# Kernel optimization log

Hardware: AMD Instinct MI355X
Metric: run time of the kernel (lower is better)

Reference implementation:

```python
import jax, jax.numpy as jnp
import numpy as np
from jax import lax

DN = ('NCHW', 'OIHW', 'NCHW')

def _conv(x, w, b, stride, pad):
    y = lax.conv_general_dilated(x, w, (stride, stride), ((pad, pad), (pad, pad)),
                                 dimension_numbers=DN)
    return y + b[None, :, None, None]

def _convT(x, w, b):
    # torch ConvTranspose2d(k=4, s=2, p=1); w: (C_in, C_out, 4, 4)
    wt = jnp.transpose(jnp.flip(w, (2, 3)), (1, 0, 2, 3))  # (C_out, C_in, 4, 4)
    y = lax.conv_general_dilated(x, wt, (1, 1), ((2, 2), (2, 2)),
                                 lhs_dilation=(2, 2), dimension_numbers=DN)
    return y + b[None, :, None, None]

def setup_inputs() -> dict:
    key = jax.random.key(0)
    ks = jax.random.split(key, 20)
    s = 0.05
    inp = {
        'x':   jax.random.normal(ks[0], (8, 1, 256, 256), jnp.float32),
        'ew1': jax.random.normal(ks[1], (64, 1, 3, 3), jnp.float32) * s,
        'eb1': jnp.zeros((64,), jnp.float32),
        'ew2': jax.random.normal(ks[2], (128, 64, 3, 3), jnp.float32) * s,
        'eb2': jnp.zeros((128,), jnp.float32),
        'ew3': jax.random.normal(ks[3], (256, 128, 3, 3), jnp.float32) * s,
        'eb3': jnp.zeros((256,), jnp.float32),
        'ew4': jax.random.normal(ks[4], (256, 256, 1, 1), jnp.float32) * s,
        'eb4': jnp.zeros((256,), jnp.float32),
        # torch init: uniform(-1/K, 1/K) with K=1024
        'codebook': jax.random.uniform(ks[5], (1024, 256), jnp.float32,
                                       minval=-1.0 / 1024, maxval=1.0 / 1024),
        'dw1': jax.random.normal(ks[6], (256, 256, 1, 1), jnp.float32) * s,
        'db1': jnp.zeros((256,), jnp.float32),
        'dw2': jax.random.normal(ks[7], (256, 128, 4, 4), jnp.float32) * s,
        'db2': jnp.zeros((128,), jnp.float32),
        'dw3': jax.random.normal(ks[8], (128, 64, 4, 4), jnp.float32) * s,
        'db3': jnp.zeros((64,), jnp.float32),
        'dw4': jax.random.normal(ks[9], (1, 64, 3, 3), jnp.float32) * s,
        'db4': jnp.zeros((1,), jnp.float32),
        'scale_idx': 2,
    }
    return inp

def reference(x, ew1, eb1, ew2, eb2, ew3, eb3, ew4, eb4, codebook,
              dw1, db1, dw2, db2, dw3, db3, dw4, db4, scale_idx):
    # ---- encoder (scale_idx=2: 1->64->128->256->embedding_dim) ----
    h = jax.nn.relu(_conv(x, ew1, eb1, 1, 1))        # [B,64,256,256]
    h = jax.nn.relu(_conv(h, ew2, eb2, 2, 1))        # [B,128,128,128]
    h = jax.nn.relu(_conv(h, ew3, eb3, 2, 1))        # [B,256,64,64]
    z = _conv(h, ew4, eb4, 1, 0)                     # [B,D,64,64]
    # ---- vector quantization ----
    B, D, H, W = z.shape
    flat = jnp.transpose(z, (0, 2, 3, 1)).reshape(-1, D)        # [N,D]
    dist = (jnp.sum(flat * flat, axis=1, keepdims=True)
            + jnp.sum(codebook * codebook, axis=1)
            - 2.0 * flat @ codebook.T)                          # [N,K]
    idx = jnp.argmin(dist, axis=1)                              # [N]
    quantized = codebook[idx].reshape(B, H, W, D)               # gather == onehot@codebook
    z_q = jnp.transpose(quantized, (0, 3, 1, 2))                # [B,D,H,W]
    indices = idx.reshape(B, H, W)
    # ---- decoder ----
    d = jax.nn.relu(_conv(z_q, dw1, db1, 1, 0))      # [B,256,64,64]
    d = jax.nn.relu(_convT(d, dw2, db2))             # [B,128,128,128]
    d = jax.nn.relu(_convT(d, dw3, db3))             # [B,64,256,256]
    recon = jax.nn.sigmoid(_conv(d, dw4, db4, 1, 1)) # [B,1,256,256]
    return recon, z_q, indices
```

## Files before the change

### kernel.cpp

```cpp
#include <hip/hip_runtime.h>
#include <hip/hip_bf16.h>
#include <math.h>


#define NB 8

typedef short v8s __attribute__((ext_vector_type(8)));
typedef float v4f __attribute__((ext_vector_type(4)));

__device__ __forceinline__ float sumsq128(const float* __restrict__ p, int stride) {
  float r[8];
#pragma unroll
  for (int j = 0; j < 8; ++j) {
    float v = p[(size_t)j * stride];
    r[j] = __fmul_rn(v, v);
  }
  for (int i = 8; i < 128; i += 8) {
#pragma unroll
    for (int j = 0; j < 8; ++j) {
      float v = p[(size_t)(i + j) * stride];
      r[j] = __fadd_rn(r[j], __fmul_rn(v, v));
    }
  }
  return __fadd_rn(__fadd_rn(__fadd_rn(r[0], r[1]), __fadd_rn(r[2], r[3])),
                   __fadd_rn(__fadd_rn(r[4], r[5]), __fadd_rn(r[6], r[7])));
}
__device__ __forceinline__ float sumsq256(const float* __restrict__ p, int stride) {
  return __fadd_rn(sumsq128(p, stride), sumsq128(p + (size_t)128 * stride, stride));
}

__global__ __launch_bounds__(256) void k_conv12(const float* __restrict__ x,
                                                const float* __restrict__ ew1,
                                                const float* __restrict__ eb1,
                                                const float* __restrict__ ew2,
                                                const float* __restrict__ bias2,
                                                float* __restrict__ out) {
  const int IH = 256;
  const int OH = 128;
  const int TILES_X = OH / 16;
  int n = blockIdx.z;
  int cg = blockIdx.y;
  int tile = blockIdx.x;
  int OY0 = (tile / TILES_X) * 16, OX0 = (tile % TILES_X) * 16;
  int ty = threadIdx.x >> 4, tx = threadIdx.x & 15;
  int oy = OY0 + ty, ox = OX0 + tx;

  const float* xin = x + (size_t)n * IH * IH;
  float xv[5][5];
#pragma unroll
  for (int a = 0; a < 5; ++a)
#pragma unroll
    for (int b = 0; b < 5; ++b) {
      int iy = 2 * oy - 2 + a, ix = 2 * ox - 2 + b;
      xv[a][b] = (iy >= 0 && iy < IH && ix >= 0 && ix < IH) ? xin[iy * IH + ix] : 0.f;
    }

  unsigned hmask = 0;
#pragma unroll
  for (int dy = 0; dy < 3; ++dy)
#pragma unroll
    for (int dx = 0; dx < 3; ++dx) {
      int hy = 2 * oy - 1 + dy, hx = 2 * ox - 1 + dx;
      if (hy >= 0 && hy < IH && hx >= 0 && hx < IH) hmask |= 1u << (dy * 3 + dx);
    }

  float acc[32];
#pragma unroll
  for (int c = 0; c < 32; ++c) acc[c] = 0.f;

  for (int ci = 0; ci < 64; ++ci) {
    const float* w1 = ew1 + ci * 9;
    float b1 = eb1[ci];
    float v[9];
#pragma unroll
    for (int dy = 0; dy < 3; ++dy)
#pragma unroll
      for (int dx = 0; dx < 3; ++dx) {
        int k = dy * 3 + dx;
        if (hmask & (1u << k)) {
          float h = b1;
#pragma unroll
          for (int ey = 0; ey < 3; ++ey)
#pragma unroll
            for (int ex = 0; ex < 3; ++ex) h += xv[dy + ey][dx + ex] * w1[ey * 3 + ex];
          v[k] = fmaxf(h, 0.f);
        } else {
          v[k] = 0.f;
        }
      }
    const float* wp = ew2 + ((size_t)(cg * 32) * 64 + ci) * 9;
#pragma unroll
    for (int c = 0; c < 32; ++c) {
#pragma unroll
      for (int k = 0; k < 9; ++k) acc[c] += v[k] * wp[(size_t)c * 64 * 9 + k];
    }
  }
  float* ob = out + (((size_t)n * 128 + cg * 32) * OH + oy) * OH + ox;
#pragma unroll
  for (int c = 0; c < 32; ++c) {
    float r = acc[c] + bias2[cg * 32 + c];
    ob[(size_t)c * OH * OH] = fmaxf(r, 0.f);
  }
}

template <int CI, int IH>
__global__ __launch_bounds__(256) void k_conv3s2(const float* __restrict__ in,
                                                 const float* __restrict__ w,
                                                 const float* __restrict__ bias,
                                                 float* __restrict__ out, int CO) {
  const int OH = IH / 2;
  const int TILES_X = OH / 16;
  const int RS = 40;
  int n = blockIdx.z;
  int cg = blockIdx.y;
  int tile = blockIdx.x;
  int OY0 = (tile / TILES_X) * 16, OX0 = (tile % TILES_X) * 16;
  int ty = threadIdx.x >> 4, tx = threadIdx.x & 15;
  __shared__ float sm[2][33 * RS];
  float acc[32];
#pragma unroll
  for (int c = 0; c < 32; ++c) acc[c] = 0.f;
  int iy0 = 2 * OY0 - 1, ix0 = 2 * OX0 - 1;
  const float* inb = in + (size_t)n * CI * IH * IH;

  for (int t = threadIdx.x; t < 2 * 33 * RS; t += 256) (&sm[0][0])[t] = 0.f;

  int goff[5], loff[5];
  unsigned vmask = 0;
#pragma unroll
  for (int i = 0; i < 5; ++i) {
    int t = threadIdx.x + 256 * i;
    if (t < 33 * 33) {
      int r = t / 33, c = t - r * 33;
      int iy = iy0 + r, ix = ix0 + c;
      if (iy >= 0 && iy < IH && ix >= 0 && ix < IH) {
        vmask |= 1u << i;
        goff[i] = iy * IH + ix;
        loff[i] = r * RS + (c >> 1) + (c & 1) * 17;
      }
    }
  }
  __syncthreads();

  auto stage = [&](int buf, int ci) {
    const float* ip = inb + (size_t)ci * IH * IH;
    float* dst = sm[buf];
#pragma unroll
    for (int i = 0; i < 5; ++i)
      if (vmask & (1u << i)) dst[loff[i]] = ip[goff[i]];
  };
  stage(0, 0);
  for (int ci = 0; ci < CI; ++ci) {
    int buf = ci & 1;
    __syncthreads();
    if (ci + 1 < CI) stage(buf ^ 1, ci + 1);
    float v[9];
#pragma unroll
    for (int dy = 0; dy < 3; ++dy)
#pragma unroll
      for (int dx = 0; dx < 3; ++dx)
        v[dy * 3 + dx] = sm[buf][(2 * ty + dy) * RS + (dx & 1) * 17 + tx + (dx >> 1)];
    const float* wp = w + ((size_t)(cg * 32) * CI + ci) * 9;
#pragma unroll
    for (int c = 0; c < 32; ++c) {
#pragma unroll
      for (int k = 0; k < 9; ++k) acc[c] += v[k] * wp[(size_t)c * CI * 9 + k];
    }
  }
  int oy = OY0 + ty, ox = OX0 + tx;
  float* ob = out + (((size_t)n * CO + cg * 32) * OH + oy) * OH + ox;
#pragma unroll
  for (int c = 0; c < 32; ++c) {
    float r = acc[c] + bias[cg * 32 + c];
    ob[(size_t)c * OH * OH] = fmaxf(r, 0.f);
  }
}

__global__ __launch_bounds__(256) void k_conv1x1(const float* __restrict__ in,
                                                 const float* __restrict__ w,
                                                 const float* __restrict__ bias,
                                                 float* __restrict__ out, int CI, int CO,
                                                 int HW) {
  int n = blockIdx.z;
  int cg = blockIdx.y;
  int px = blockIdx.x * 256 + threadIdx.x;
  __shared__ float sm[16][256];
  const float* inb = in + (size_t)n * CI * HW;
  float acc[8];
#pragma unroll
  for (int c = 0; c < 8; ++c) acc[c] = 0.f;
  for (int c0 = 0; c0 < CI; c0 += 16) {
#pragma unroll
    for (int i = 0; i < 16; ++i) sm[i][threadIdx.x] = inb[(size_t)(c0 + i) * HW + px];
    __syncthreads();
    const float* wb = w + (size_t)(cg * 8) * CI + c0;
#pragma unroll
    for (int i = 0; i < 16; ++i) {
      float r = sm[i][threadIdx.x];
#pragma unroll
      for (int c = 0; c < 8; ++c) acc[c] += r * wb[(size_t)c * CI + i];
    }
    __syncthreads();
  }
#pragma unroll
  for (int c = 0; c < 8; ++c) {
    float r = acc[c] + bias[cg * 8 + c];
    out[((size_t)n * CO + cg * 8 + c) * HW + px] = r;
  }
}

__global__ __launch_bounds__(256) void k_cnorm(const float* __restrict__ cb,
                                               float* __restrict__ cn) {
  int j = blockIdx.x * 256 + threadIdx.x;
  if (j < 1024) cn[j] = sumsq256(cb + (size_t)j * 256, 1);
}

__global__ __launch_bounds__(256) void k_xnorm(const float* __restrict__ z,
                                               float* __restrict__ xn) {
  int t = blockIdx.x * 256 + threadIdx.x;
  int n = t >> 12, yx = t & 4095;
  xn[t] = sumsq256(z + (size_t)n * 256 * 4096 + yx, 4096);
}

__global__ __launch_bounds__(256) void k_vq(const float* __restrict__ z,
                                            const float* __restrict__ cb,
                                            const float* __restrict__ cn,
                                            const float* __restrict__ xn,
                                            int* __restrict__ idx,
                                            float* __restrict__ idxf) {
  __shared__ __align__(16) float zt[64][68];
  __shared__ float ct[64][65];
  __shared__ float cnt[64];
  __shared__ float xnt[64];
  __shared__ float rbest[64][17];
  __shared__ int ribest[64][17];
  int tid = threadIdx.x;
  int pq = tid & 15;
  int cq = tid >> 4;
  int p0 = blockIdx.x * 64;
  int n = p0 >> 12;
  int yx0 = p0 & 4095;
  const float* zb = z + (size_t)n * 256 * 4096 + yx0;
  if (tid < 64) xnt[tid] = xn[p0 + tid];
  float best[4] = {3.0e38f, 3.0e38f, 3.0e38f, 3.0e38f};
  int bidx[4] = {0, 0, 0, 0};
  for (int c0 = 0; c0 < 1024; c0 += 64) {
    float acc[4][4];
#pragma unroll
    for (int a = 0; a < 4; ++a)
#pragma unroll
      for (int b = 0; b < 4; ++b) acc[a][b] = 0.f;
    for (int k0 = 0; k0 < 256; k0 += 64) {
      __syncthreads();
      for (int t = tid; t < 4096; t += 256) {
        int r = t >> 6, c = t & 63;
        zt[r][c] = zb[(size_t)(k0 + r) * 4096 + c];
      }
      for (int t = tid; t < 4096; t += 256) {
        int c = t >> 6, r = t & 63;
        ct[c][r] = cb[(size_t)(c0 + c) * 256 + k0 + r];
      }
      if (k0 == 0 && tid < 64) cnt[tid] = cn[c0 + tid];
      __syncthreads();
#pragma unroll 8
      for (int k = 0; k < 64; ++k) {
        const float4 zz = *reinterpret_cast<const float4*>(&zt[k][pq * 4]);
#pragma unroll
        for (int j = 0; j < 4; ++j) {
          float cv = ct[cq * 4 + j][k];
          acc[0][j] += zz.x * cv;
          acc[1][j] += zz.y * cv;
          acc[2][j] += zz.z * cv;
          acc[3][j] += zz.w * cv;
        }
      }
    }
#pragma unroll
    for (int pi = 0; pi < 4; ++pi) {
      float xnp = xnt[pq * 4 + pi];
#pragma unroll
      for (int j = 0; j < 4; ++j) {
        float A = __fadd_rn(xnp, cnt[cq * 4 + j]);
        float d = __fsub_rn(A, __fmul_rn(2.0f, acc[pi][j]));
        if (d < best[pi]) {
          best[pi] = d;
          bidx[pi] = c0 + cq * 4 + j;
        }
      }
    }
  }
  __syncthreads();
#pragma unroll
  for (int pi = 0; pi < 4; ++pi) {
    rbest[pq * 4 + pi][cq] = best[pi];
    ribest[pq * 4 + pi][cq] = bidx[pi];
  }
  __syncthreads();
  if (tid < 64) {
    float bv = rbest[tid][0];
    int bj = ribest[tid][0];
    for (int g = 1; g < 16; ++g) {
      float v = rbest[tid][g];
      int j2 = ribest[tid][g];
      if (v < bv || (v == bv && j2 < bj)) { bv = v; bj = j2; }
    }
    idx[p0 + tid] = bj;
    idxf[p0 + tid] = (float)bj;
  }
}

__global__ __launch_bounds__(256) void k_gather(const int* __restrict__ idx,
                                                const float* __restrict__ cb,
                                                float* __restrict__ zq,
                                                __hip_bfloat16* __restrict__ zqbf) {
  size_t t = (size_t)blockIdx.x * 256 + threadIdx.x;
  int yx = (int)(t & 4095);
  int d = (int)((t >> 12) & 255);
  int n = (int)(t >> 20);
  int p = (n << 12) | yx;
  float v = cb[(size_t)idx[p] * 256 + d];
  zq[t] = v;
  zqbf[t] = __float2bfloat16(v);
}

__global__ __launch_bounds__(256) void k_wconv(const float* __restrict__ w,
                                               __hip_bfloat16* __restrict__ wA,
                                               int CI, int CO) {
  int t = blockIdx.x * 256 + threadIdx.x;
  int total = 4 * CO * CI * 4;
  if (t >= total) return;
  int tap = t & 3;
  int q = t >> 2;
  int ci = q % CI;
  int pc = q / CI;
  int co = pc % CO;
  int par = pc / CO;
  int a = tap >> 1, b = tap & 1, ry = par >> 1, rx = par & 1;
  float v = w[((size_t)ci * CO + co) * 16 + (3 - ry - 2 * a) * 4 + (3 - rx - 2 * b)];
  wA[t] = __float2bfloat16(v);
}

__global__ __launch_bounds__(256) void k_wconv1(const float* __restrict__ w,
                                                __hip_bfloat16* __restrict__ wb) {
  int t = blockIdx.x * 256 + threadIdx.x;
  if (t < 65536) wb[t] = __float2bfloat16(w[t]);
}

__global__ __launch_bounds__(256) void k_d1mfma(const __hip_bfloat16* __restrict__ in,
                                                const __hip_bfloat16* __restrict__ wb,
                                                const float* __restrict__ bias,
                                                __hip_bfloat16* __restrict__ out) {
  int n = blockIdx.z;
  int co0 = blockIdx.y * 64;
  int px0 = blockIdx.x * 64;
  int tid = threadIdx.x;
  int w = tid >> 6, lane = tid & 63, fr = lane & 15, kg = lane >> 4;

  __shared__ __align__(16) ushort Wt[64][40];
  __shared__ __align__(16) ushort Zt[64][40];

  v4f acc[4];
#pragma unroll
  for (int q = 0; q < 4; ++q) acc[q] = (v4f){0.f, 0.f, 0.f, 0.f};

  const ushort* inb = (const ushort*)in + (size_t)n * 256 * 4096;
  const ushort* wab = (const ushort*)wb;

  for (int k0 = 0; k0 < 256; k0 += 32) {
    __syncthreads();
    {
      int co = tid & 63, kgg = tid >> 6;
      const uint4 v = *(const uint4*)(wab + (size_t)(co0 + co) * 256 + k0 + kgg * 8);
      *(uint4*)&Wt[co][kgg * 8] = v;
    }
    {
      int ci = tid >> 3, pxg = tid & 7;
      const ushort* src = inb + (size_t)(k0 + ci) * 4096 + px0 + pxg * 8;
      uint4 v = *(const uint4*)src;
      const ushort* vs = (const ushort*)&v;
#pragma unroll
      for (int j = 0; j < 8; ++j) Zt[pxg * 8 + j][ci] = vs[j];
    }
    __syncthreads();
    v8s af = *(const v8s*)&Wt[w * 16 + fr][kg * 8];
#pragma unroll
    for (int q = 0; q < 4; ++q) {
      v8s b = *(const v8s*)&Zt[q * 16 + fr][kg * 8];
      acc[q] = __builtin_amdgcn_mfma_f32_16x16x32_bf16(af, b, acc[q], 0, 0, 0);
    }
  }
  __hip_bfloat16* ob = out + (size_t)n * 256 * 4096;
#pragma unroll
  for (int q = 0; q < 4; ++q) {
    int px = px0 + q * 16 + fr;
#pragma unroll
    for (int r = 0; r < 4; ++r) {
      int co = co0 + w * 16 + kg * 4 + r;
      float val = fmaxf(acc[q][r] + bias[co], 0.f);
      ob[(size_t)co * 4096 + px] = __float2bfloat16(val);
    }
  }
}

template <int CI, int IH, int CO>
__global__ __launch_bounds__(256) void k_convTmfma(const __hip_bfloat16* __restrict__ in,
                                                   const __hip_bfloat16* __restrict__ wA,
                                                   const float* __restrict__ bias,
                                                   __hip_bfloat16* __restrict__ out) {
  const int OH = 2 * IH;
  const int NT = IH / 32;
  int n = blockIdx.z;
  int co0 = blockIdx.y * 64;
  int m = blockIdx.x / NT;
  int n0x = (blockIdx.x % NT) * 32;
  int tid = threadIdx.x;
  int w = tid >> 6, lane = tid & 63, fr = lane & 15, kg = lane >> 4;

  __shared__ __align__(16) ushort Wt[4][64][40];
  __shared__ __align__(16) ushort Bt[4][32][40];
  __shared__ ushort patch[8][3][36];

  v4f acc[4][2];
#pragma unroll
  for (int p = 0; p < 4; ++p)
#pragma unroll
    for (int h = 0; h < 2; ++h) acc[p][h] = (v4f){0.f, 0.f, 0.f, 0.f};

  const ushort* inb = (const ushort*)in + (size_t)n * CI * IH * IH;
  const ushort* wab = (const ushort*)wA;

  for (int t = tid; t < 8 * 3 * 36; t += 256) (&patch[0][0][0])[t] = 0;

  int pgoff[4], ploff[4];
  unsigned pmask = 0;
#pragma unroll
  for (int i = 0; i < 4; ++i) {
    int t = tid + 256 * i;
    if (t < 816) {
      int ci = t / 102;
      int rem = t - ci * 102;
      int r = rem / 34;
      int c = rem - r * 34;
      int iy = m - 1 + r, ix = n0x - 1 + c;
      if (iy >= 0 && iy < IH && ix >= 0 && ix < IH) {
        pmask |= 1u << i;
        pgoff[i] = (ci * IH + iy) * IH + ix;
        ploff[i] = (ci * 3 + r) * 36 + c;
      }
    }
  }

  for (int ci0 = 0; ci0 < CI; ci0 += 8) {
    __syncthreads();
    {
      const ushort* ip = inb + (size_t)ci0 * IH * IH;
      ushort* pb = &patch[0][0][0];
#pragma unroll
      for (int i = 0; i < 4; ++i)
        if (pmask & (1u << i)) pb[ploff[i]] = ip[pgoff[i]];
    }
#pragma unroll
    for (int i = 0; i < 4; ++i) {
      int u = tid + 256 * i;
      int kgg = u & 3, co = (u >> 2) & 63, par = u >> 8;
      const uint4 v =
          *(const uint4*)(wab + (((size_t)par * CO + co0 + co) * CI + ci0) * 4 + kgg * 8);
      *(uint4*)&Wt[par][co][kgg * 8] = v;
    }
    __syncthreads();
    {
      int pr = tid >> 1;
      int px0 = (tid & 1) * 16;
      int par = pr >> 5, k = pr & 31;
      int ci = k >> 2, a = (k >> 1) & 1, b = k & 1, ry = par >> 1, rx = par & 1;
      const ushort* src = &patch[ci][ry + a][px0 + rx + b];
      ushort* dst = &Bt[par][px0][k];
#pragma unroll
      for (int p = 0; p < 16; ++p) dst[p * 40] = src[p];
    }
    __syncthreads();
#pragma unroll
    for (int par = 0; par < 4; ++par) {
      v8s af = *(const v8s*)&Wt[par][w * 16 + fr][kg * 8];
      v8s b0 = *(const v8s*)&Bt[par][fr][kg * 8];
      v8s b1 = *(const v8s*)&Bt[par][16 + fr][kg * 8];
      acc[par][0] = __builtin_amdgcn_mfma_f32_16x16x32_bf16(af, b0, acc[par][0], 0, 0, 0);
      acc[par][1] = __builtin_amdgcn_mfma_f32_16x16x32_bf16(af, b1, acc[par][1], 0, 0, 0);
    }
  }
  __hip_bfloat16* ob = out + (size_t)n * CO * OH * OH;
#pragma unroll
  for (int par = 0; par < 4; ++par) {
    int ry = par >> 1, rx = par & 1;
    int oy = 2 * m + ry;
#pragma unroll
    for (int h = 0; h < 2; ++h) {
      int ox = 2 * (n0x + h * 16 + fr) + rx;
#pragma unroll
      for (int r = 0; r < 4; ++r) {
        int co = co0 + w * 16 + kg * 4 + r;
        float val = acc[par][h][r] + bias[co];
        val = fmaxf(val, 0.f);
        ob[((size_t)co * OH + oy) * OH + ox] = __float2bfloat16(val);
      }
    }
  }
}

__global__ __launch_bounds__(256) void k_conv_out(const __hip_bfloat16* __restrict__ in,
                                                  const float* __restrict__ w,
                                                  const float* __restrict__ bias,
                                                  float* __restrict__ out) {
  int n = blockIdx.z;
  int tile = blockIdx.x;
  int TY0 = (tile / 16) * 16, TX0 = (tile % 16) * 16;
  int ty = threadIdx.x >> 4, tx = threadIdx.x & 15;
  __shared__ float sm[2][18 * 18];
  float acc = bias[0];
  const __hip_bfloat16* inb = in + (size_t)n * 64 * 65536;
  int goff[2], loff[2];
  unsigned vmask = 0;
#pragma unroll
  for (int i = 0; i < 2; ++i) {
    int t = threadIdx.x + 256 * i;
    if (t < 324) {
      int r = t / 18, c = t - r * 18;
      int iy = TY0 - 1 + r, ix = TX0 - 1 + c;
      if (iy >= 0 && iy < 256 && ix >= 0 && ix < 256) {
        vmask |= 1u << i;
        goff[i] = iy * 256 + ix;
        loff[i] = t;
      }
    }
  }
  for (int t = threadIdx.x; t < 2 * 324; t += 256) (&sm[0][0])[t] = 0.f;
  __syncthreads();
  auto stage = [&](int buf, int ci) {
    const __hip_bfloat16* ip = inb + (size_t)ci * 65536;
    float* dst = sm[buf];
#pragma unroll
    for (int i = 0; i < 2; ++i)
      if (vmask & (1u << i)) dst[loff[i]] = __bfloat162float(ip[goff[i]]);
  };
  stage(0, 0);
  for (int ci = 0; ci < 64; ++ci) {
    int buf = ci & 1;
    __syncthreads();
    if (ci + 1 < 64) stage(buf ^ 1, ci + 1);
    const float* wp = w + ci * 9;
#pragma unroll
    for (int dy = 0; dy < 3; ++dy)
#pragma unroll
      for (int dx = 0; dx < 3; ++dx) acc += sm[buf][(ty + dy) * 18 + tx + dx] * wp[dy * 3 + dx];
  }
  out[(size_t)n * 65536 + (TY0 + ty) * 256 + TX0 + tx] = 1.f / (1.f + expf(-acc));
}

extern "C" void kernel_launch(void* const* d_in, const int* in_sizes, int n_in,
                              void* d_out, int out_size, void* d_ws, size_t ws_size,
                              hipStream_t stream) {
  const float* x = (const float*)d_in[0];
  const float* ew1 = (const float*)d_in[1];
  const float* eb1 = (const float*)d_in[2];
  const float* ew2 = (const float*)d_in[3];
  const float* eb2 = (const float*)d_in[4];
  const float* ew3 = (const float*)d_in[5];
  const float* eb3 = (const float*)d_in[6];
  const float* ew4 = (const float*)d_in[7];
  const float* eb4 = (const float*)d_in[8];
  const float* cb = (const float*)d_in[9];
  const float* dw1 = (const float*)d_in[10];
  const float* db1 = (const float*)d_in[11];
  const float* dw2 = (const float*)d_in[12];
  const float* db2 = (const float*)d_in[13];
  const float* dw3 = (const float*)d_in[14];
  const float* db3 = (const float*)d_in[15];
  const float* dw4 = (const float*)d_in[16];
  const float* db4 = (const float*)d_in[17];

  float* ws = (float*)d_ws;
  float* A = ws;
  float* Bb = ws + 33554432;
  float* Cc = ws + 50331648;
  float* cn = A + 16777216;
  float* xn = A + 16778240;
  int* idx = (int*)(A + 16811008);
  __hip_bfloat16* zqbf = (__hip_bfloat16*)(A + 20971520);
  __hip_bfloat16* wbfA2 = (__hip_bfloat16*)(A + 25165824);
  __hip_bfloat16* wbfA3 = (__hip_bfloat16*)(A + 25427968);
  __hip_bfloat16* wbf1 = (__hip_bfloat16*)(A + 25493504);
  __hip_bfloat16* d1bf = (__hip_bfloat16*)Cc;
  __hip_bfloat16* d2bf = (__hip_bfloat16*)Bb;
  __hip_bfloat16* d3bf = (__hip_bfloat16*)A;

  float* recon = (float*)d_out;
  float* zq = recon + 524288;
  float* idxf = zq + 8388608;

  k_conv12<<<dim3(64, 4, NB), 256, 0, stream>>>(x, ew1, eb1, ew2, eb2, Bb);
  k_conv3s2<128, 128><<<dim3(16, 8, NB), 256, 0, stream>>>(Bb, ew3, eb3, Cc, 256);
  k_conv1x1<<<dim3(16, 32, NB), 256, 0, stream>>>(Cc, ew4, eb4, A, 256, 256, 4096);
  k_wconv<<<2048, 256, 0, stream>>>(dw2, wbfA2, 256, 128);
  k_wconv<<<512, 256, 0, stream>>>(dw3, wbfA3, 128, 64);
  k_wconv1<<<256, 256, 0, stream>>>(dw1, wbf1);
  k_cnorm<<<4, 256, 0, stream>>>(cb, cn);
  k_xnorm<<<128, 256, 0, stream>>>(A, xn);
  k_vq<<<512, 256, 0, stream>>>(A, cb, cn, xn, idx, idxf);
  k_gather<<<32768, 256, 0, stream>>>(idx, cb, zq, zqbf);
  k_d1mfma<<<dim3(64, 4, NB), 256, 0, stream>>>(zqbf, wbf1, db1, d1bf);
  k_convTmfma<256, 64, 128><<<dim3(128, 2, NB), 256, 0, stream>>>(d1bf, wbfA2, db2, d2bf);
  k_convTmfma<128, 128, 64><<<dim3(512, 1, NB), 256, 0, stream>>>(d2bf, wbfA3, db3, d3bf);
  k_conv_out<<<dim3(256, 1, NB), 256, 0, stream>>>(d3bf, dw4, db4, recon);
}
```

Baseline: 1.845 ms.

## Increase register tiling in conv1x1, VQ distance loop, and output conv

Three kernels get larger per-thread work. conv1x1 now computes 16 output channels per thread instead of 8 and launches half the blocks. The VQ inner loop reads the codebook tile with float4 loads, padding the tile row to 68 floats, and does a 4x4 register outer product per step. The final 3x3 conv computes a 2x2 output patch per thread from a 4x4 register window over a 32x32 tile. The aim is to cut shared and global load traffic per FMA, at the cost of more registers and fewer blocks.

```diff
diff --git a/kernel.cpp b/kernel.cpp
--- a/kernel.cpp
+++ b/kernel.cpp
@@ -186,26 +186,26 @@
   int px = blockIdx.x * 256 + threadIdx.x;
   __shared__ float sm[16][256];
   const float* inb = in + (size_t)n * CI * HW;
-  float acc[8];
-#pragma unroll
-  for (int c = 0; c < 8; ++c) acc[c] = 0.f;
+  float acc[16];
+#pragma unroll
+  for (int c = 0; c < 16; ++c) acc[c] = 0.f;
   for (int c0 = 0; c0 < CI; c0 += 16) {
 #pragma unroll
     for (int i = 0; i < 16; ++i) sm[i][threadIdx.x] = inb[(size_t)(c0 + i) * HW + px];
     __syncthreads();
-    const float* wb = w + (size_t)(cg * 8) * CI + c0;
+    const float* wb = w + (size_t)(cg * 16) * CI + c0;
 #pragma unroll
     for (int i = 0; i < 16; ++i) {
       float r = sm[i][threadIdx.x];
 #pragma unroll
-      for (int c = 0; c < 8; ++c) acc[c] += r * wb[(size_t)c * CI + i];
-    }
-    __syncthreads();
-  }
-#pragma unroll
-  for (int c = 0; c < 8; ++c) {
-    float r = acc[c] + bias[cg * 8 + c];
-    out[((size_t)n * CO + cg * 8 + c) * HW + px] = r;
+      for (int c = 0; c < 16; ++c) acc[c] += r * wb[(size_t)c * CI + i];
+    }
+    __syncthreads();
+  }
+#pragma unroll
+  for (int c = 0; c < 16; ++c) {
+    float r = acc[c] + bias[cg * 16 + c];
+    out[((size_t)n * CO + cg * 16 + c) * HW + px] = r;
   }
 }
 
@@ -229,7 +229,7 @@
                                             int* __restrict__ idx,
                                             float* __restrict__ idxf) {
   __shared__ __align__(16) float zt[64][68];
-  __shared__ float ct[64][65];
+  __shared__ __align__(16) float ct[64][68];
   __shared__ float cnt[64];
   __shared__ float xnt[64];
   __shared__ float rbest[64][17];
@@ -262,16 +262,24 @@
       }
       if (k0 == 0 && tid < 64) cnt[tid] = cn[c0 + tid];
       __syncthreads();
-#pragma unroll 8
-      for (int k = 0; k < 64; ++k) {
-        const float4 zz = *reinterpret_cast<const float4*>(&zt[k][pq * 4]);
-#pragma unroll
-        for (int j = 0; j < 4; ++j) {
-          float cv = ct[cq * 4 + j][k];
-          acc[0][j] += zz.x * cv;
-          acc[1][j] += zz.y * cv;
-          acc[2][j] += zz.z * cv;
-          acc[3][j] += zz.w * cv;
+#pragma unroll 4
+      for (int k = 0; k < 64; k += 4) {
+        float4 za[4];
+#pragma unroll
+        for (int i = 0; i < 4; ++i) za[i] = *(const float4*)&zt[k + i][pq * 4];
+        float4 cv[4];
+#pragma unroll
+        for (int j = 0; j < 4; ++j) cv[j] = *(const float4*)&ct[cq * 4 + j][k];
+#pragma unroll
+        for (int i = 0; i < 4; ++i) {
+#pragma unroll
+          for (int j = 0; j < 4; ++j) {
+            float cvi = (i == 0) ? cv[j].x : (i == 1) ? cv[j].y : (i == 2) ? cv[j].z : cv[j].w;
+            acc[0][j] += za[i].x * cvi;
+            acc[1][j] += za[i].y * cvi;
+            acc[2][j] += za[i].z * cvi;
+            acc[3][j] += za[i].w * cvi;
+          }
         }
       }
     }
@@ -513,33 +521,39 @@
                                                   float* __restrict__ out) {
   int n = blockIdx.z;
   int tile = blockIdx.x;
-  int TY0 = (tile / 16) * 16, TX0 = (tile % 16) * 16;
+  int TY0 = (tile >> 3) * 32, TX0 = (tile & 7) * 32;
   int ty = threadIdx.x >> 4, tx = threadIdx.x & 15;
-  __shared__ float sm[2][18 * 18];
-  float acc = bias[0];
+  __shared__ float sm[2][34 * 36];
+  float acc[4];
+  float b0 = bias[0];
+#pragma unroll
+  for (int p = 0; p < 4; ++p) acc[p] = b0;
   const __hip_bfloat16* inb = in + (size_t)n * 64 * 65536;
-  int goff[2], loff[2];
+
+  for (int t = threadIdx.x; t < 2 * 34 * 36; t += 256) (&sm[0][0])[t] = 0.f;
+
+  int goff[5], loff[5];
   unsigned vmask = 0;
 #pragma unroll
-  for (int i = 0; i < 2; ++i) {
+  for (int i = 0; i < 5; ++i) {
     int t = threadIdx.x + 256 * i;
-    if (t < 324) {
-      int r = t / 18, c = t - r * 18;
+    if (t < 34 * 34) {
+      int r = t / 34, c = t - r * 34;
       int iy = TY0 - 1 + r, ix = TX0 - 1 + c;
       if (iy >= 0 && iy < 256 && ix >= 0 && ix < 256) {
         vmask |= 1u << i;
         goff[i] = iy * 256 + ix;
-        loff[i] = t;
-      }
-    }
-  }
-  for (int t = threadIdx.x; t < 2 * 324; t += 256) (&sm[0][0])[t] = 0.f;
+        loff[i] = r * 36 + c;
+      }
+    }
+  }
   __syncthreads();
+
   auto stage = [&](int buf, int ci) {
     const __hip_bfloat16* ip = inb + (size_t)ci * 65536;
     float* dst = sm[buf];
 #pragma unroll
-    for (int i = 0; i < 2; ++i)
+    for (int i = 0; i < 5; ++i)
       if (vmask & (1u << i)) dst[loff[i]] = __bfloat162float(ip[goff[i]]);
   };
   stage(0, 0);
@@ -547,13 +561,31 @@
     int buf = ci & 1;
     __syncthreads();
     if (ci + 1 < 64) stage(buf ^ 1, ci + 1);
+    float w4[4][4];
+#pragma unroll
+    for (int a = 0; a < 4; ++a)
+#pragma unroll
+      for (int b = 0; b < 4; ++b) w4[a][b] = sm[buf][(2 * ty + a) * 36 + 2 * tx + b];
     const float* wp = w + ci * 9;
 #pragma unroll
     for (int dy = 0; dy < 3; ++dy)
 #pragma unroll
-      for (int dx = 0; dx < 3; ++dx) acc += sm[buf][(ty + dy) * 18 + tx + dx] * wp[dy * 3 + dx];
-  }
-  out[(size_t)n * 65536 + (TY0 + ty) * 256 + TX0 + tx] = 1.f / (1.f + expf(-acc));
+      for (int dx = 0; dx < 3; ++dx) {
+        float wv = wp[dy * 3 + dx];
+        acc[0] += w4[dy][dx] * wv;
+        acc[1] += w4[dy][dx + 1] * wv;
+        acc[2] += w4[dy + 1][dx] * wv;
+        acc[3] += w4[dy + 1][dx + 1] * wv;
+      }
+  }
+  float* ob = out + (size_t)n * 65536 + (TY0 + 2 * ty) * 256 + TX0 + 2 * tx;
+#pragma unroll
+  for (int py = 0; py < 2; ++py) {
+    float2 v2;
+    v2.x = 1.f / (1.f + expf(-acc[py * 2 + 0]));
+    v2.y = 1.f / (1.f + expf(-acc[py * 2 + 1]));
+    *reinterpret_cast<float2*>(ob + (size_t)py * 256) = v2;
+  }
 }
 
 extern "C" void kernel_launch(void* const* d_in, const int* in_sizes, int n_in,
@@ -599,7 +631,7 @@
 
   k_conv12<<<dim3(64, 4, NB), 256, 0, stream>>>(x, ew1, eb1, ew2, eb2, Bb);
   k_conv3s2<128, 128><<<dim3(16, 8, NB), 256, 0, stream>>>(Bb, ew3, eb3, Cc, 256);
-  k_conv1x1<<<dim3(16, 32, NB), 256, 0, stream>>>(Cc, ew4, eb4, A, 256, 256, 4096);
+  k_conv1x1<<<dim3(16, 16, NB), 256, 0, stream>>>(Cc, ew4, eb4, A, 256, 256, 4096);
   k_wconv<<<2048, 256, 0, stream>>>(dw2, wbfA2, 256, 128);
   k_wconv<<<512, 256, 0, stream>>>(dw3, wbfA3, 128, 64);
   k_wconv1<<<256, 256, 0, stream>>>(dw1, wbf1);
@@ -610,5 +642,5 @@
   k_d1mfma<<<dim3(64, 4, NB), 256, 0, stream>>>(zqbf, wbf1, db1, d1bf);
   k_convTmfma<256, 64, 128><<<dim3(128, 2, NB), 256, 0, stream>>>(d1bf, wbfA2, db2, d2bf);
   k_convTmfma<128, 128, 64><<<dim3(512, 1, NB), 256, 0, stream>>>(d2bf, wbfA3, db3, d3bf);
-  k_conv_out<<<dim3(256, 1, NB), 256, 0, stream>>>(d3bf, dw4, db4, recon);
-}
+  k_conv_out<<<dim3(64, 1, NB), 256, 0, stream>>>(d3bf, dw4, db4, recon);
+}
```

Result: slower. 1.957 ms (+6.1%).
